# Performance work log

Measured on AMD Instinct MI355X. Metric: run time of the kernel, lower is better.

## Reference

```python
import jax, jax.numpy as jnp
import numpy as np

THRESHOLD = 0.5
PSI_ZONE = 0.1


def dequantize_ternary(w, threshold=THRESHOLD, psi_zone=PSI_ZONE):
    """Faithful reproduction of TernaryTensor.from_float followed by to_float.

    Branch order matches the original code:
      v > threshold        -> +1
      v < -threshold       -> -1
      |v| < psi_zone       -> 0
      otherwise (PSI)      -> (v + threshold) / (2 * threshold)  (stored psi_prob)
    """
    psi_val = (w + threshold) / (2.0 * threshold)
    return jnp.where(
        w > threshold, 1.0,
        jnp.where(
            w < -threshold, -1.0,
            jnp.where(jnp.abs(w) < psi_zone, 0.0, psi_val),
        ),
    ).astype(w.dtype)


def setup_inputs() -> dict:
    key = jax.random.key(0)
    k_x, k_w = jax.random.split(key)
    batch, in_features, out_features = 8192, 4096, 4096
    x = jax.random.normal(k_x, (batch, in_features), dtype=jnp.float32)
    # original: torch.randn(out, in) * 0.1
    weight_float = jax.random.normal(k_w, (out_features, in_features), dtype=jnp.float32) * 0.1
    bias = jnp.zeros((out_features,), dtype=jnp.float32)
    return {"x": x, "weight_float": weight_float, "bias": bias}


def reference(x, weight_float, bias):
    w = dequantize_ternary(weight_float)  # [out, in]
    return jnp.matmul(x, w.T) + bias      # [batch, out]
```

## Files before the change

kernel.cpp:

```cpp
#include <hip/hip_runtime.h>
#include <stdint.h>

#define THRESH 0.5f
#define PSI 0.1f

typedef short bfrag_t __attribute__((ext_vector_type(8)));
typedef float f32x16 __attribute__((ext_vector_type(16)));
typedef unsigned short u16x8 __attribute__((ext_vector_type(8)));

#define GLD16(gsrc, ldst)                                                                \
    __builtin_amdgcn_global_load_lds((const __attribute__((address_space(1))) void*)(gsrc), \
                                     (__attribute__((address_space(3))) void*)(ldst),       \
                                     16, 0, 0)

#define WAITVM(n)   asm volatile("s_waitcnt vmcnt(" #n ")" ::: "memory")
#define WAITLGKM(n) asm volatile("s_waitcnt lgkmcnt(" #n ")" ::: "memory")
#define SB()        __builtin_amdgcn_sched_barrier(0)
#define BAR()                                  \
    do {                                       \
        asm volatile("" ::: "memory");         \
        __builtin_amdgcn_s_barrier();          \
        asm volatile("" ::: "memory");         \
    } while (0)

__device__ __forceinline__ float dequant(float v) {
    if (v > THRESH) return 1.0f;
    if (v < -THRESH) return -1.0f;
    if (fabsf(v) < PSI) return 0.0f;
    return (v + THRESH) / (2.0f * THRESH);
}

__device__ __forceinline__ unsigned short f2bf(float f) {
    unsigned int u = __float_as_uint(f);
    u += 0x7FFFu + ((u >> 16) & 1u);
    return (unsigned short)(u >> 16);
}

template <bool DO_DEQUANT>
__global__ void pack_kernel(const float* __restrict__ src, unsigned short* __restrict__ dst, int K) {
    __shared__ char lsm[16384];
    const int t   = threadIdx.x;
    const int nkc = K >> 8;
    const int b   = blockIdx.x / nkc;
    const int kc  = blockIdx.x % nkc;
    const int k0  = kc << 8;
    const int r   = t >> 3;
    const int j   = t & 7;

    const float4* s4 = (const float4*)(src + (size_t)((b << 5) + r) * K + k0 + (j << 5));
    float4 f[8];
#pragma unroll
    for (int i = 0; i < 8; ++i) f[i] = s4[i];

#pragma unroll
    for (int gi = 0; gi < 4; ++gi) {
        float4 lo = f[2 * gi], hi4 = f[2 * gi + 1];
        u16x8 o;
        if (DO_DEQUANT) {
            o[0] = f2bf(dequant(lo.x));  o[1] = f2bf(dequant(lo.y));
            o[2] = f2bf(dequant(lo.z));  o[3] = f2bf(dequant(lo.w));
            o[4] = f2bf(dequant(hi4.x)); o[5] = f2bf(dequant(hi4.y));
            o[6] = f2bf(dequant(hi4.z)); o[7] = f2bf(dequant(hi4.w));
        } else {
            o[0] = f2bf(lo.x);  o[1] = f2bf(lo.y);  o[2] = f2bf(lo.z);  o[3] = f2bf(lo.w);
            o[4] = f2bf(hi4.x); o[5] = f2bf(hi4.y); o[6] = f2bf(hi4.z); o[7] = f2bf(hi4.w);
        }
        const int S_rel = 2 * j + (gi >> 1);
        const int slot  = ((gi & 1) << 5) + r;
        *(u16x8*)(lsm + S_rel * 1024 + slot * 16) = o;
    }
    __syncthreads();

    unsigned short* gdst = dst + (((size_t)b * (K >> 4) + (kc << 4)) << 9) + (size_t)t * 32;
#pragma unroll
    for (int i = 0; i < 4; ++i)
        *(u16x8*)(gdst + i * 8) = *(const u16x8*)(lsm + t * 64 + i * 16);
}


__device__ __forceinline__ bfrag_t rdfrag32(const char* halfBase, int band, int ks, int l16) {
    return *(const bfrag_t*)(halfBase + (band << 11) + (ks << 10) + l16);
}

__global__ __launch_bounds__(512, 2) void gemm256p_kernel(
        const unsigned short* __restrict__ Ap,
        const unsigned short* __restrict__ Bp,
        const float* __restrict__ bias,
        float* __restrict__ C,
        int M, int N, int K) {
    __shared__ char ldsB[131072];

    const int t    = threadIdx.x;
    const int w    = t >> 6;
    const int l    = t & 63;
    const int wr   = w >> 2;
    const int wc   = w & 3;
    const int lr32 = l & 31;
    const int hi   = l >> 5;
    const int l16  = l << 4;

    const int nwg = gridDim.x;
    int bid = blockIdx.x;
    if ((nwg & 7) == 0) bid = (bid & 7) * (nwg >> 3) + (bid >> 3);
    const int nbn  = N >> 8;
    const int brow = (bid / nbn) << 8;
    const int bcol = (bid % nbn) << 8;

    const int Kc = K >> 4;
    const char* pA = (const char*)Ap + (((size_t)(((brow >> 5) + w) * (size_t)Kc)) << 10) + l16;
    const char* pB = (const char*)Bp + (((size_t)(((bcol >> 5) + w) * (size_t)Kc)) << 10) + l16;
    const int c16a = w * 2 + 0, c16b = w * 2 + 1;

#define STAGE_A(buf, half, kE)                                                              \
    do {                                                                                    \
        const size_t so_ = ((size_t)(((kE) >> 4) + (half) * 2)) << 10;                      \
        GLD16(pA + so_,        ldsB + (buf) * 65536 + (half) * 16384 + c16a * 1024);        \
        GLD16(pA + so_ + 1024, ldsB + (buf) * 65536 + (half) * 16384 + c16b * 1024);        \
    } while (0)
#define STAGE_B(buf, half, kE)                                                              \
    do {                                                                                    \
        const size_t so_ = ((size_t)(((kE) >> 4) + (half) * 2)) << 10;                      \
        GLD16(pB + so_,        ldsB + (buf) * 65536 + 32768 + (half) * 16384 + c16a * 1024);\
        GLD16(pB + so_ + 1024, ldsB + (buf) * 65536 + 32768 + (half) * 16384 + c16b * 1024);\
    } while (0)

#define QMFMA(qm, bq, nn)                                                                 \
    do {                                                                                  \
        __builtin_amdgcn_s_setprio(1);                                                    \
        _Pragma("unroll") for (int ks = 0; ks < 4; ++ks)                                  \
        _Pragma("unroll") for (int mi = 0; mi < 2; ++mi)                                  \
            acc[(qm) * 2 + mi][nn] = __builtin_amdgcn_mfma_f32_32x32x16_bf16(             \
                a[mi][ks], bq[ks], acc[(qm) * 2 + mi][nn], 0, 0, 0);                      \
        __builtin_amdgcn_s_setprio(0);                                                    \
    } while (0)

    f32x16 acc[4][2];
#pragma unroll
    for (int m = 0; m < 4; ++m)
#pragma unroll
        for (int n = 0; n < 2; ++n)
#pragma unroll
            for (int r = 0; r < 16; ++r)
                acc[m][n][r] = 0.f;

    const int NT = K >> 6;
    const int wrB4 = wr << 2;
    const int wcB2 = wc << 1;

    STAGE_A(0, 0, 0);  STAGE_A(0, 1, 0);
    STAGE_B(0, 0, 0);  STAGE_B(0, 1, 0);
    STAGE_B(1, 0, 64); STAGE_B(1, 1, 64);
    WAITVM(4);
    BAR();

    bfrag_t a[2][4], b0[4], b1[4];

#define TILE(tv, XO, YO, Xb, Yb)                                                          \
    do {                                                                                  \
        int t1_ = (tv) + 1; if (t1_ >= NT) t1_ -= NT;              \
        int t2_ = (tv) + 2; if (t2_ >= NT) t2_ -= NT;                                     \
        const char* aH0 = ldsB + (XO);                                                    \
        const char* aH1 = aH0 + 16384;                                                    \
        const char* bH0 = aH0 + 32768;                                                    \
        const char* bH1 = aH0 + 49152;                                                    \
        const int kY1 = t1_ << 6, kX2 = t2_ << 6;                                         \
                                                \
        _Pragma("unroll") for (int mi = 0; mi < 2; ++mi)                                  \
        _Pragma("unroll") for (int ks = 0; ks < 4; ++ks)                                  \
            a[mi][ks] = rdfrag32(ks < 2 ? aH0 : aH1, wrB4 + mi, ks & 1, l16);             \
        _Pragma("unroll") for (int ks = 0; ks < 4; ++ks)                                  \
            b0[ks] = rdfrag32(ks < 2 ? bH0 : bH1, wcB2 + 0, ks & 1, l16);                 \
        SB();                                                                             \
                                                                  \
        _Pragma("unroll") for (int ks = 0; ks < 4; ++ks)                                  \
            b1[ks] = rdfrag32(ks < 2 ? bH0 : bH1, wcB2 + 1, ks & 1, l16);                 \
        SB();                                                                             \
        STAGE_A(Yb, 0, kY1); STAGE_A(Yb, 1, kY1);                                         \
        WAITLGKM(4); SB();                          \
        QMFMA(0, b0, 0);                                                                  \
        WAITLGKM(0); SB();                                                   \
        QMFMA(0, b1, 1);                                                                  \
                              \
        _Pragma("unroll") for (int mi = 0; mi < 2; ++mi)                                  \
        _Pragma("unroll") for (int ks = 0; ks < 4; ++ks)                                  \
            a[mi][ks] = rdfrag32(ks < 2 ? aH0 : aH1, wrB4 + 2 + mi, ks & 1, l16);         \
        SB();                                                                             \
        BAR();                        \
        STAGE_B(Xb, 0, kX2); STAGE_B(Xb, 1, kX2);                                         \
        WAITLGKM(0); SB();                                              \
        QMFMA(1, b1, 1);                                                                  \
        QMFMA(1, b0, 0);                                                                  \
        WAITVM(4);                            \
        BAR();                                                             \
    } while (0)

    for (int tt = 0; tt < NT; tt += 2) {
        TILE(tt,     0,     65536, 0, 1);
        TILE(tt + 1, 65536, 0,     1, 0);
    }

    WAITVM(0);

    float bv[2];
#pragma unroll
    for (int nn = 0; nn < 2; ++nn) bv[nn] = bias[bcol + (wc << 6) + nn * 32 + lr32];
#pragma unroll
    for (int mm = 0; mm < 4; ++mm) {
#pragma unroll
        for (int nn = 0; nn < 2; ++nn) {
            const int gc = bcol + (wc << 6) + nn * 32 + lr32;
#pragma unroll
            for (int reg = 0; reg < 16; ++reg) {
                const int row = (reg & 3) + 8 * (reg >> 2) + 4 * hi;
                C[(size_t)(brow + (wr << 7) + mm * 32 + row) * N + gc] = acc[mm][nn][reg] + bv[nn];
            }
        }
    }
    (void)M;
#undef STAGE_A
#undef STAGE_B
#undef QMFMA
#undef TILE
}

__global__ void gemm_fallback_kernel(const float* __restrict__ X, const float* __restrict__ W,
                                     const float* __restrict__ bias, float* __restrict__ C,
                                     int M, int N, int K) {
    __shared__ float sX[16][17];
    __shared__ float sW[16][17];
    const int tx = threadIdx.x & 15;
    const int ty = threadIdx.x >> 4;
    const int row = blockIdx.y * 16 + ty;
    const int colBase = blockIdx.x * 16;
    const int col = colBase + tx;
    float acc = 0.f;
    for (int k0 = 0; k0 < K; k0 += 16) {
        sX[ty][tx] = (row < M && k0 + tx < K) ? X[(size_t)row * K + k0 + tx] : 0.f;
        const int wrow = colBase + ty;
        sW[ty][tx] = (wrow < N && k0 + tx < K) ? dequant(W[(size_t)wrow * K + k0 + tx]) : 0.f;
        __syncthreads();
#pragma unroll
        for (int kk = 0; kk < 16; ++kk)
            acc += sX[ty][kk] * sW[tx][kk];
        __syncthreads();
    }
    if (row < M && col < N)
        C[(size_t)row * N + col] = acc + bias[col];
}

extern "C" void kernel_launch(void* const* d_in, const int* in_sizes, int n_in,
                              void* d_out, int out_size, void* d_ws, size_t ws_size,
                              hipStream_t stream) {
    const float* x    = (const float*)d_in[0];
    const float* w    = (const float*)d_in[1];
    const float* bias = (const float*)d_in[2];
    float* out        = (float*)d_out;

    const int N = in_sizes[2];
    const int K = in_sizes[1] / N;
    const int M = in_sizes[0] / K;

    const size_t need = ((size_t)M * K + (size_t)N * K) * sizeof(unsigned short);
    const bool fast = (ws_size >= need) && (M % 256 == 0) && (N % 256 == 0) &&
                      (K % 256 == 0);

    if (fast) {
        unsigned short* xp = (unsigned short*)d_ws;
        unsigned short* wp = xp + (size_t)M * K;
        pack_kernel<false><<<dim3((M / 32) * (K / 256)), dim3(256), 0, stream>>>(x, xp, K);
        pack_kernel<true ><<<dim3((N / 32) * (K / 256)), dim3(256), 0, stream>>>(w, wp, K);
        gemm256p_kernel<<<dim3((M / 256) * (N / 256)), dim3(512), 0, stream>>>(xp, wp, bias, out, M, N, K);
    } else {
        dim3 g((N + 15) / 16, (M + 15) / 16);
        gemm_fallback_kernel<<<g, dim3(256), 0, stream>>>(x, w, bias, out, M, N, K);
    }
    (void)n_in; (void)out_size;
}
```

Before: 301.0 us.

## Load B fragments directly from global into registers, stage only A in LDS

The GEMM kernel stops staging B tiles in LDS. Each wave now loads its own B fragments from global memory straight into registers, prefetched one K-tile ahead, and only A stays double-buffered in LDS, which halves LDS use to 64KB. The goal is to cut LDS traffic and footprint and to drop the B LDS write/read round trip. The cost is higher register pressure and redundant global B loads across the waves that share B columns, and the vmcnt/barrier accounting also changes with the new load mix.

```diff
diff --git a/kernel.cpp b/kernel.cpp
--- a/kernel.cpp
+++ b/kernel.cpp
@@ -78,17 +78,13 @@
 }
 
 
-__device__ __forceinline__ bfrag_t rdfrag32(const char* halfBase, int band, int ks, int l16) {
-    return *(const bfrag_t*)(halfBase + (band << 11) + (ks << 10) + l16);
-}
-
-__global__ __launch_bounds__(512, 2) void gemm256p_kernel(
+__global__ __launch_bounds__(512, 2) void gemm256r_kernel(
         const unsigned short* __restrict__ Ap,
         const unsigned short* __restrict__ Bp,
         const float* __restrict__ bias,
         float* __restrict__ C,
         int M, int N, int K) {
-    __shared__ char ldsB[131072];
+    __shared__ char ldsB[65536];
 
     const int t    = threadIdx.x;
     const int w    = t >> 6;
@@ -107,31 +103,42 @@
     const int bcol = (bid % nbn) << 8;
 
     const int Kc = K >> 4;
-    const char* pA = (const char*)Ap + (((size_t)(((brow >> 5) + w) * (size_t)Kc)) << 10) + l16;
-    const char* pB = (const char*)Bp + (((size_t)(((bcol >> 5) + w) * (size_t)Kc)) << 10) + l16;
-    const int c16a = w * 2 + 0, c16b = w * 2 + 1;
-
-#define STAGE_A(buf, half, kE)                                                              \
-    do {                                                                                    \
-        const size_t so_ = ((size_t)(((kE) >> 4) + (half) * 2)) << 10;                      \
-        GLD16(pA + so_,        ldsB + (buf) * 65536 + (half) * 16384 + c16a * 1024);        \
-        GLD16(pA + so_ + 1024, ldsB + (buf) * 65536 + (half) * 16384 + c16b * 1024);        \
-    } while (0)
-#define STAGE_B(buf, half, kE)                                                              \
-    do {                                                                                    \
-        const size_t so_ = ((size_t)(((kE) >> 4) + (half) * 2)) << 10;                      \
-        GLD16(pB + so_,        ldsB + (buf) * 65536 + 32768 + (half) * 16384 + c16a * 1024);\
-        GLD16(pB + so_ + 1024, ldsB + (buf) * 65536 + 32768 + (half) * 16384 + c16b * 1024);\
-    } while (0)
-
-#define QMFMA(qm, bq, nn)                                                                 \
-    do {                                                                                  \
-        __builtin_amdgcn_s_setprio(1);                                                    \
-        _Pragma("unroll") for (int ks = 0; ks < 4; ++ks)                                  \
-        _Pragma("unroll") for (int mi = 0; mi < 2; ++mi)                                  \
-            acc[(qm) * 2 + mi][nn] = __builtin_amdgcn_mfma_f32_32x32x16_bf16(             \
-                a[mi][ks], bq[ks], acc[(qm) * 2 + mi][nn], 0, 0, 0);                      \
-        __builtin_amdgcn_s_setprio(0);                                                    \
+    const char* pA  = (const char*)Ap + ((((size_t)((brow >> 5) + w)) * Kc) << 10) + l16;
+    const char* pB0 = (const char*)Bp + ((((size_t)((bcol >> 5) + (wc << 1))) * Kc) << 10) + l16;
+    const char* pB1 = pB0 + ((size_t)Kc << 10);
+    const int c16a = w * 2, c16b = w * 2 + 1;
+
+#define STAGE_A4(bufO, tv)                                                     \
+    do {                                                                       \
+        const size_t s0_ = ((size_t)(tv) << 12);                               \
+        GLD16(pA + s0_,        ldsB + (bufO) + c16a * 1024);                   \
+        GLD16(pA + s0_ + 1024, ldsB + (bufO) + c16b * 1024);                   \
+        GLD16(pA + s0_ + 2048, ldsB + (bufO) + 16384 + c16a * 1024);           \
+        GLD16(pA + s0_ + 3072, ldsB + (bufO) + 16384 + c16b * 1024);           \
+    } while (0)
+
+#define RDA(XO, mi, ksa)                                                       \
+    (*(const bfrag_t*)(ldsB + (XO) + (((ksa) >> 1) << 14) +                    \
+                       (((wr << 2) + (mi)) << 11) + (((ksa) & 1) << 10) + l16))
+
+#define LDB(Vv, tb)                                                            \
+    do {                                                                       \
+        _Pragma("unroll") for (int ks = 0; ks < 4; ++ks) {                     \
+            Vv##0[ks] = *(const bfrag_t*)(pB0 + ((((size_t)(tb) << 2) + ks) << 10)); \
+            Vv##1[ks] = *(const bfrag_t*)(pB1 + ((((size_t)(tb) << 2) + ks) << 10)); \
+        }                                                                      \
+    } while (0)
+
+#define MFMA8(ar, Uv, ks)                                                      \
+    do {                                                                       \
+        __builtin_amdgcn_s_setprio(1);                                         \
+        _Pragma("unroll") for (int mi = 0; mi < 4; ++mi) {                     \
+            acc[mi][0] = __builtin_amdgcn_mfma_f32_32x32x16_bf16(              \
+                ar[mi], Uv##0[ks], acc[mi][0], 0, 0, 0);                       \
+            acc[mi][1] = __builtin_amdgcn_mfma_f32_32x32x16_bf16(              \
+                ar[mi], Uv##1[ks], acc[mi][1], 0, 0, 0);                       \
+        }                                                                      \
+        __builtin_amdgcn_s_setprio(0);                                         \
     } while (0)
 
     f32x16 acc[4][2];
@@ -144,59 +151,43 @@
                 acc[m][n][r] = 0.f;
 
     const int NT = K >> 6;
-    const int wrB4 = wr << 2;
-    const int wcB2 = wc << 1;
-
-    STAGE_A(0, 0, 0);  STAGE_A(0, 1, 0);
-    STAGE_B(0, 0, 0);  STAGE_B(0, 1, 0);
-    STAGE_B(1, 0, 64); STAGE_B(1, 1, 64);
+
+    bfrag_t U0[4], U1[4], V0[4], V1[4], aP[4], aQ[4];
+
+    STAGE_A4(0, 0);
+    LDB(U, 0);
+    STAGE_A4(32768, 1);
     WAITVM(4);
     BAR();
 
-    bfrag_t a[2][4], b0[4], b1[4];
-
-#define TILE(tv, XO, YO, Xb, Yb)                                                          \
-    do {                                                                                  \
-        int t1_ = (tv) + 1; if (t1_ >= NT) t1_ -= NT;              \
-        int t2_ = (tv) + 2; if (t2_ >= NT) t2_ -= NT;                                     \
-        const char* aH0 = ldsB + (XO);                                                    \
-        const char* aH1 = aH0 + 16384;                                                    \
-        const char* bH0 = aH0 + 32768;                                                    \
-        const char* bH1 = aH0 + 49152;                                                    \
-        const int kY1 = t1_ << 6, kX2 = t2_ << 6;                                         \
-                                                \
-        _Pragma("unroll") for (int mi = 0; mi < 2; ++mi)                                  \
-        _Pragma("unroll") for (int ks = 0; ks < 4; ++ks)                                  \
-            a[mi][ks] = rdfrag32(ks < 2 ? aH0 : aH1, wrB4 + mi, ks & 1, l16);             \
-        _Pragma("unroll") for (int ks = 0; ks < 4; ++ks)                                  \
-            b0[ks] = rdfrag32(ks < 2 ? bH0 : bH1, wcB2 + 0, ks & 1, l16);                 \
-        SB();                                                                             \
-                                                                  \
-        _Pragma("unroll") for (int ks = 0; ks < 4; ++ks)                                  \
-            b1[ks] = rdfrag32(ks < 2 ? bH0 : bH1, wcB2 + 1, ks & 1, l16);                 \
-        SB();                                                                             \
-        STAGE_A(Yb, 0, kY1); STAGE_A(Yb, 1, kY1);                                         \
-        WAITLGKM(4); SB();                          \
-        QMFMA(0, b0, 0);                                                                  \
-        WAITLGKM(0); SB();                                                   \
-        QMFMA(0, b1, 1);                                                                  \
-                              \
-        _Pragma("unroll") for (int mi = 0; mi < 2; ++mi)                                  \
-        _Pragma("unroll") for (int ks = 0; ks < 4; ++ks)                                  \
-            a[mi][ks] = rdfrag32(ks < 2 ? aH0 : aH1, wrB4 + 2 + mi, ks & 1, l16);         \
-        SB();                                                                             \
-        BAR();                        \
-        STAGE_B(Xb, 0, kX2); STAGE_B(Xb, 1, kX2);                                         \
-        WAITLGKM(0); SB();                                              \
-        QMFMA(1, b1, 1);                                                                  \
-        QMFMA(1, b0, 0);                                                                  \
-        WAITVM(4);                            \
-        BAR();                                                             \
+#define TILE(tv, XO, Ucur, Vnxt)                                               \
+    do {                                                                       \
+        int t1_ = (tv) + 1; if (t1_ >= NT) t1_ -= NT;   \
+        int t2_ = (tv) + 2; if (t2_ >= NT) t2_ -= NT;                          \
+        _Pragma("unroll") for (int mi = 0; mi < 4; ++mi) aP[mi] = RDA(XO, mi, 0); \
+        SB();                                                                  \
+        LDB(Vnxt, t1_);          \
+        SB();                                                                  \
+        _Pragma("unroll") for (int mi = 0; mi < 4; ++mi) aQ[mi] = RDA(XO, mi, 1); \
+        SB(); WAITLGKM(4); SB();        \
+        MFMA8(aP, Ucur, 0);                                                    \
+        _Pragma("unroll") for (int mi = 0; mi < 4; ++mi) aP[mi] = RDA(XO, mi, 2); \
+        SB(); WAITLGKM(4); SB();                                               \
+        MFMA8(aQ, Ucur, 1);                                                    \
+        _Pragma("unroll") for (int mi = 0; mi < 4; ++mi) aQ[mi] = RDA(XO, mi, 3); \
+        SB(); WAITLGKM(4); SB();                                               \
+        MFMA8(aP, Ucur, 2);                                                    \
+        WAITLGKM(0); SB();             \
+        BAR();                           \
+        STAGE_A4(XO, t2_);                                                     \
+        MFMA8(aQ, Ucur, 3);                                                    \
+        WAITVM(4);                \
+        BAR();                                             \
     } while (0)
 
     for (int tt = 0; tt < NT; tt += 2) {
-        TILE(tt,     0,     65536, 0, 1);
-        TILE(tt + 1, 65536, 0,     1, 0);
+        TILE(tt,     0,     U, V);
+        TILE(tt + 1, 32768, V, U);
     }
 
     WAITVM(0);
@@ -217,9 +208,10 @@
         }
     }
     (void)M;
-#undef STAGE_A
-#undef STAGE_B
-#undef QMFMA
+#undef STAGE_A4
+#undef RDA
+#undef LDB
+#undef MFMA8
 #undef TILE
 }
 
@@ -269,7 +261,7 @@
         unsigned short* wp = xp + (size_t)M * K;
         pack_kernel<false><<<dim3((M / 32) * (K / 256)), dim3(256), 0, stream>>>(x, xp, K);
         pack_kernel<true ><<<dim3((N / 32) * (K / 256)), dim3(256), 0, stream>>>(w, wp, K);
-        gemm256p_kernel<<<dim3((M / 256) * (N / 256)), dim3(512), 0, stream>>>(xp, wp, bias, out, M, N, K);
+        gemm256r_kernel<<<dim3((M / 256) * (N / 256)), dim3(512), 0, stream>>>(xp, wp, bias, out, M, N, K);
     } else {
         dim3 g((N + 15) / 16, (M + 15) / 16);
         gemm_fallback_kernel<<<g, dim3(256), 0, stream>>>(x, w, bias, out, M, N, K);
```

After: 300.4 us. No clear change (-0.2%).
